# Kernel optimization log

Measured on AMD Instinct MI355X. Metric: run time of the kernel, lower is better.

Reference implementation:

```python
import jax, jax.numpy as jnp
import numpy as np

SCORE_THRESH = 0.05
NMS_THRESH = 0.5
DETS_PER_IMG = 100
IMG_W, IMG_H = 1333.0, 800.0
BBOX_XFORM_CLIP = float(np.log(1000.0 / 16.0))
WX, WY, WW, WH = 10.0, 10.0, 5.0, 5.0


def decode_boxes(rel, ref):
    widths = ref[:, 2] - ref[:, 0] + 1.0
    heights = ref[:, 3] - ref[:, 1] + 1.0
    ctr_x = ref[:, 0] + 0.5 * widths
    ctr_y = ref[:, 1] + 0.5 * heights
    dx = rel[:, 0] / WX
    dy = rel[:, 1] / WY
    dw = jnp.minimum(rel[:, 2] / WW, BBOX_XFORM_CLIP)
    dh = jnp.minimum(rel[:, 3] / WH, BBOX_XFORM_CLIP)
    pcx = dx * widths + ctr_x
    pcy = dy * heights + ctr_y
    pw = jnp.exp(dw) * widths
    ph = jnp.exp(dh) * heights
    return jnp.stack([pcx - 0.5 * pw, pcy - 0.5 * ph,
                      pcx + 0.5 * pw - 1.0, pcy + 0.5 * ph - 1.0], axis=1)


def pairwise_iou(b):
    # torchvision-style IoU (no +1), b: [n,4] xyxy
    area = (b[:, 2] - b[:, 0]) * (b[:, 3] - b[:, 1])
    lt = jnp.maximum(b[:, None, :2], b[None, :, :2])
    rb = jnp.minimum(b[:, None, 2:], b[None, :, 2:])
    wh = jnp.clip(rb - lt, 0.0)
    inter = wh[..., 0] * wh[..., 1]
    return inter / (area[:, None] + area[None, :] - inter + 1e-12)


def nms_keep(boxes, scores, valid):
    # masked greedy NMS; returns boolean keep mask in original order
    n = boxes.shape[0]
    order = jnp.argsort(-jnp.where(valid, scores, -jnp.inf))
    b = boxes[order]
    v = valid[order]
    iou = pairwise_iou(b)  # [n,n]
    idx = jnp.arange(n)

    def body(i, keep):
        suppressed = jnp.any(keep & (iou[i] > NMS_THRESH) & (idx < i))
        return keep.at[i].set(v[i] & ~suppressed)

    keep_sorted = jax.lax.fori_loop(0, n, body, jnp.zeros(n, dtype=bool))
    return jnp.zeros(n, dtype=bool).at[order].set(keep_sorted)


def setup_inputs() -> dict:
    key = jax.random.key(0)
    k1, k2, k3, k4, k5 = jax.random.split(key, 5)
    C, K = 16, 2048
    class_logit = jax.random.normal(k1, (C * K, 2), jnp.float32)
    box_regression = jax.random.normal(k2, (C * K, 8), jnp.float32) * 0.5
    x1 = jax.random.uniform(k3, (K,)) * (IMG_W - 220.0)
    y1 = jax.random.uniform(k4, (K,)) * (IMG_H - 220.0)
    wh = 20.0 + jax.random.uniform(k5, (K, 2)) * 180.0
    proposal_boxes = jnp.stack([x1, y1, x1 + wh[:, 0], y1 + wh[:, 1]], axis=1).astype(jnp.float32)
    unique_labels = jnp.arange(1, C + 1, dtype=jnp.int32)
    return {"class_logit": class_logit, "box_regression": box_regression,
            "proposal_boxes": proposal_boxes, "unique_labels": unique_labels}


def reference(class_logit, box_regression, proposal_boxes, unique_labels):
    C = unique_labels.shape[0]
    K = proposal_boxes.shape[0]
    # softmax over binary logits, take foreground prob
    prob = jax.nn.softmax(class_logit, axis=1)[:, 1]  # [C*K]
    rel = box_regression[:, 4:8]
    ref_boxes = jnp.tile(proposal_boxes, (C, 1))  # class-major [C*K,4]
    dec = decode_boxes(rel, ref_boxes)
    # clip_to_image (remove_empty=False), TO_REMOVE = 1
    dec = jnp.stack([jnp.clip(dec[:, 0], 0.0, IMG_W - 1.0),
                     jnp.clip(dec[:, 1], 0.0, IMG_H - 1.0),
                     jnp.clip(dec[:, 2], 0.0, IMG_W - 1.0),
                     jnp.clip(dec[:, 3], 0.0, IMG_H - 1.0)], axis=1)
    boxes_c = dec.reshape(C, K, 4)
    scores_c = prob.reshape(C, K)
    valid = scores_c > SCORE_THRESH
    keep = jax.vmap(nms_keep)(boxes_c, scores_c, valid).reshape(-1)  # [C*K]
    flat_scores = scores_c.reshape(-1)
    n_det = jnp.sum(keep)
    masked = jnp.where(keep, flat_scores, -jnp.inf)
    kth = jax.lax.top_k(masked, DETS_PER_IMG)[0][-1]  # 100th largest kept score
    keep_final = jnp.where(n_det > DETS_PER_IMG, keep & (flat_scores >= kth), keep)
    labels = jnp.broadcast_to(unique_labels[:, None], (C, K)).reshape(-1)
    out_boxes = jnp.where(keep_final[:, None], dec, 0.0)
    out_scores = jnp.where(keep_final, flat_scores, 0.0)
    out5 = jnp.concatenate([out_boxes, out_scores[:, None]], axis=1)  # [C*K,5]
    return out5, labels, keep_final
```

## Files before the change

### kernel.cpp

```cpp
#include <hip/hip_runtime.h>
#include <hip/hip_bf16.h>

#define NCLS 16
#define NBOX 2048
#define NTOT (NCLS * NBOX)
#define NCHUNK 32
#define SCORE_THRESH 0.05f
#define NMS_THRESH 0.5f
#define DETS_PER_IMG 100
#define TOPC 128
#define BBOX_CLIP 4.135166556742356f

typedef unsigned long long u64;

__device__ __forceinline__ u64 sel_mx(u64 a, u64 b, bool keepmax) {
    u64 mx = (a > b) ? a : b;
    u64 mn = (a > b) ? b : a;
    return keepmax ? mx : mn;
}

__global__ __launch_bounds__(1024) void sortmask_kernel(
    const float* __restrict__ logits,
    const float* __restrict__ regr,
    const float* __restrict__ props,
    float4* __restrict__ dec,
    u64* __restrict__ keys_out,
    u64* __restrict__ maskT)
{
    int blk = blockIdx.x;
    int c = blk >> 4;
    int p = blk & 15;
    int tid = threadIdx.x;

    int w = tid >> 6, l = tid & 63;
    int p0 = w * 128 + l;
    int p1 = p0 + 64;
    __shared__ float4 decv[NBOX];
    __shared__ float4 boxu[NBOX];
    u64* sk = (u64*)boxu;
    float4* box = boxu;

    u64 e01[2];
#pragma unroll
    for (int s = 0; s < 2; s++) {
#pragma clang fp contract(off)
        int t = s ? p1 : p0;
        int i = c * NBOX + t;
        float x0 = logits[2 * i + 0];
        float x1 = logits[2 * i + 1];
        float m = fmaxf(x0, x1);
        float e0f = expf(x0 - m);
        float e1f = expf(x1 - m);
        float score = e1f / (e0f + e1f);

        float px1 = props[4 * t + 0];
        float py1 = props[4 * t + 1];
        float px2 = props[4 * t + 2];
        float py2 = props[4 * t + 3];

        float bw = px2 - px1 + 1.0f;
        float bh = py2 - py1 + 1.0f;
        float cx = px1 + 0.5f * bw;
        float cy = py1 + 0.5f * bh;

        float dx = regr[8 * i + 4] / 10.0f;
        float dy = regr[8 * i + 5] / 10.0f;
        float dw = fminf(regr[8 * i + 6] / 5.0f, BBOX_CLIP);
        float dh = fminf(regr[8 * i + 7] / 5.0f, BBOX_CLIP);

        float pcx = dx * bw + cx;
        float pcy = dy * bh + cy;
        float pw  = expf(dw) * bw;
        float ph  = expf(dh) * bh;

        float b0 = pcx - 0.5f * pw;
        float b1 = pcy - 0.5f * ph;
        float b2 = pcx + 0.5f * pw - 1.0f;
        float b3 = pcy + 0.5f * ph - 1.0f;

        b0 = fminf(fmaxf(b0, 0.0f), 1332.0f);
        b1 = fminf(fmaxf(b1, 0.0f), 799.0f);
        b2 = fminf(fmaxf(b2, 0.0f), 1332.0f);
        b3 = fminf(fmaxf(b3, 0.0f), 799.0f);

        float4 bb = make_float4(b0, b1, b2, b3);
        decv[t] = bb;
        if (p == 0) dec[i] = bb;

        unsigned mono = 0u;
        if (score > SCORE_THRESH) mono = __float_as_uint(score) | 0x80000000u;
        e01[s] = ((u64)mono << 32) | (u64)(unsigned)(NBOX - 1 - t);
    }
    u64 e0 = e01[0], e1 = e01[1];

    for (int k = 2; k <= NBOX; k <<= 1) {
        bool desc0 = (p0 & k) == 0;
        bool desc1 = (p1 & k) == 0;
        for (int j = k >> 1; j > 0; j >>= 1) {
            if (j >= 128) {
                sk[p0] = e0; sk[p1] = e1;
                __syncthreads();
                u64 q0 = sk[p0 ^ j];
                u64 q1 = sk[p1 ^ j];
                e0 = sel_mx(e0, q0, desc0 ^ ((p0 & j) != 0));
                e1 = sel_mx(e1, q1, desc1 ^ ((p1 & j) != 0));
                __syncthreads();
            } else if (j == 64) {
                u64 mx = (e0 > e1) ? e0 : e1;
                u64 mn = (e0 > e1) ? e1 : e0;
                e0 = desc0 ? mx : mn;
                e1 = desc0 ? mn : mx;
            } else {
                u64 q0 = __shfl_xor(e0, j);
                u64 q1 = __shfl_xor(e1, j);
                bool hi = (l & j) != 0;
                e0 = sel_mx(e0, q0, desc0 ^ hi);
                e1 = sel_mx(e1, q1, desc1 ^ hi);
            }
        }
    }

    sk[p0] = e0; sk[p1] = e1;
    __syncthreads();

    u64 k0 = sk[tid];
    u64 k1 = sk[tid + 1024];
    if (p == 0) {
        keys_out[c * NBOX + tid] = k0;
        keys_out[c * NBOX + tid + 1024] = k1;
    }
    int i0 = (NBOX - 1) - (int)(k0 & 0xFFFFFFFFull);
    int i1 = (NBOX - 1) - (int)(k1 & 0xFFFFFFFFull);
    float4 g0 = decv[i0];
    float4 g1 = decv[i1];
    __syncthreads();
    box[tid] = g0;
    box[tid + 1024] = g1;
    __syncthreads();

    int r = tid & 63;
    int g = tid >> 6;

    for (int pass = 0; pass < 2; pass++) {
#pragma clang fp contract(off)
        int Jc = pass ? (31 - p) : p;
        int j = Jc * 64 + r;
        float4 jb = box[j];
        float jar = (jb.z - jb.x) * (jb.w - jb.y);
        float hj = 0.5f * jar;
        float colC = hj + 5e-13f;

        for (int I = g; I <= Jc; I += 16) {
            u64 wm = 0;
            int rbase = I * 64;
#pragma unroll
            for (int i2 = 0; i2 < 64; i2++) {
#pragma clang fp contract(off)
                int gi = rbase + i2;
                float4 rb = box[gi];
                float ar = (rb.z - rb.x) * (rb.w - rb.y);
                float rha = 0.5f * ar;
                float lx = fmaxf(rb.x, jb.x);
                float ly = fmaxf(rb.y, jb.y);
                float rx = fminf(rb.z, jb.z);
                float ry = fminf(rb.w, jb.w);
                float ww = fmaxf(rx - lx, 0.0f);
                float hh = fmaxf(ry - ly, 0.0f);
                float inter = ww * hh;
                float s  = rha + colC;
                float band = 2e-6f * s;
                float delta = fmaf(1.5f, inter, -s);
                bool over = delta > band;
                bool amb = fabsf(delta) <= band;
                if (__any(amb)) {
                    float un = ar + jar - inter + 1e-12f;
                    float iou = inter / un;
                    bool ovx = iou > NMS_THRESH;
                    over = amb ? ovx : over;
                }
                if (over) wm |= 1ull << i2;
            }
            if (I == Jc) wm &= (1ull << r) - 1ull;
            maskT[((size_t)c * NCHUNK + I) * NBOX + j] = wm;
        }
    }
}

__global__ __launch_bounds__(64) void resolve_kernel(
    const u64* __restrict__ keys,
    const u64* __restrict__ maskT,
    unsigned* __restrict__ keepbits,
    unsigned* __restrict__ compact,
    int* __restrict__ nkept)
{
    int c = blockIdx.x;
    int l = threadIdx.x;
    const u64* MT = maskT + (size_t)c * NCHUNK * NBOX;
    const u64* K  = keys + (size_t)c * NBOX;

    unsigned sup = 0;
    int offset = 0;
    u64 tm[2][NCHUNK - 1];

#pragma unroll
    for (int t = 0; t < NCHUNK - 1; t++)
        tm[0][t] = MT[(size_t)(1 + t) * 64 + l];
    u64 diag = MT[l];
    u64 key  = K[l];

#pragma unroll
    for (int I = 0; I < NCHUNK; I++) {
        u64 diagN = diag, keyN = key;
        if (I + 1 < NCHUNK) {
            const u64* rowpN = MT + (size_t)(I + 1) * NBOX + l;
#pragma unroll
            for (int t = 0; t < NCHUNK - 2 - I; t++)
                tm[(I + 1) & 1][t] = rowpN[(size_t)(I + 2 + t) * 64];
            diagN = MT[(size_t)(I + 1) * NBOX + (size_t)(I + 1) * 64 + l];
            keyN  = K[(I + 1) * 64 + l];
        }
        __builtin_amdgcn_sched_barrier(0);

        unsigned mono = (unsigned)(key >> 32);
        bool av = (mono != 0u) && (((sup >> I) & 1u) == 0u);
        u64 kept = 0;
        u64 availB = __ballot(av);
        while (availB) {
            u64 front = __ballot(av && ((diag & availB) == 0ull));
            kept |= front;
            bool fr = ((front >> l) & 1ull) != 0ull;
            bool sp = ((diag & front) != 0ull);
            av = av && !fr && !sp;
            availB = __ballot(av);
        }

        int idx = (NBOX - 1) - (int)(key & 0xFFFFFFFFull);
        bool isk = ((kept >> l) & 1ull) != 0ull;
        keepbits[c * NBOX + idx] = isk ? (mono & 0x7FFFFFFFu) : 0u;

        int pos = offset + __popcll(kept & ((1ull << l) - 1ull));
        if (isk && pos < TOPC) compact[c * TOPC + pos] = mono;
        offset += __popcll(kept);

#pragma unroll
        for (int t = 0; t < NCHUNK - 1 - I; t++)
            sup |= (tm[I & 1][t] & kept) ? (1u << (I + 1 + t)) : 0u;

        diag = diagN;
        key  = keyN;
    }

    for (int t = offset + l; t < TOPC; t += 64) compact[c * TOPC + t] = 0u;
    if (l == 0) nkept[c] = offset;
}

__global__ __launch_bounds__(256) void selectwrite_kernel(
    const unsigned* __restrict__ compact,
    const int* __restrict__ nkept,
    const unsigned* __restrict__ keepbits,
    const float4* __restrict__ dec,
    const int* __restrict__ ulabels,
    float* __restrict__ out)
{
    __shared__ unsigned ls[NCLS * TOPC];
    __shared__ int s_stats[2];
    int tid = threadIdx.x;

    for (int t = tid; t < NCLS * TOPC; t += 256) ls[t] = compact[t];
    __syncthreads();

    if (tid < 64) {
        int l = tid;
        int n_c = (l < NCLS) ? nkept[l] : 0;
        int nd = n_c;
#pragma unroll
        for (int off = 32; off > 0; off >>= 1) nd += __shfl_down(nd, off);
        nd = __shfl(nd, 0);

        unsigned kth = 0u;
        if (nd > DETS_PER_IMG) {
            const unsigned* my = &ls[(l & 15) * TOPC];
            bool active = (l < NCLS);
            unsigned prefix = 0u;
            for (int bit = 31; bit >= 0; bit--) {
                unsigned cand = prefix | (1u << bit);
                int cnt = 0;
                if (active) {
                    if (my[TOPC - 1] >= cand) cnt = TOPC;
                    else {
                        int pos = 0;
#pragma unroll
                        for (int step = 64; step >= 1; step >>= 1)
                            if (my[pos + step - 1] >= cand) pos += step;
                        cnt = pos;
                    }
                }
#pragma unroll
                for (int off = 32; off > 0; off >>= 1) cnt += __shfl_down(cnt, off);
                cnt = __shfl(cnt, 0);
                if (cnt >= DETS_PER_IMG) prefix = cand;
            }
            kth = prefix & 0x7FFFFFFFu;
        }
        if (l == 0) { s_stats[0] = nd; s_stats[1] = (int)kth; }
    }
    __syncthreads();

    int n_det = s_stats[0];
    unsigned kth = (unsigned)s_stats[1];

    int i = blockIdx.x * 256 + tid;
    unsigned kb = keepbits[i];
    bool kf = kb && (n_det <= DETS_PER_IMG || kb >= kth);

    float4 b = dec[i];
    float* o5 = out + (size_t)i * 5;
    if (kf) {
        o5[0] = b.x; o5[1] = b.y; o5[2] = b.z; o5[3] = b.w;
        o5[4] = __uint_as_float(kb);
    } else {
        o5[0] = 0.0f; o5[1] = 0.0f; o5[2] = 0.0f; o5[3] = 0.0f; o5[4] = 0.0f;
    }

    int c = i >> 11;
    out[NTOT * 5 + i] = (float)ulabels[c];
    out[NTOT * 5 + NTOT + i] = kf ? 1.0f : 0.0f;
}

extern "C" void kernel_launch(void* const* d_in, const int* in_sizes, int n_in,
                              void* d_out, int out_size, void* d_ws, size_t ws_size,
                              hipStream_t stream) {
    (void)in_sizes; (void)n_in; (void)out_size; (void)ws_size;

    const float* class_logit    = (const float*)d_in[0];
    const float* box_regression = (const float*)d_in[1];
    const float* proposal_boxes = (const float*)d_in[2];
    const int*   unique_labels  = (const int*)d_in[3];

    char* ws = (char*)d_ws;
    float4* dec        = (float4*)(ws + 0);
    u64* keys          = (u64*)(ws + 524288);
    u64* maskT         = (u64*)(ws + 786432);
    unsigned* keepbits = (unsigned*)(ws + 9175040);
    unsigned* compact  = (unsigned*)(ws + 9306112);
    int* nkept         = (int*)(ws + 9314304);

    float* out = (float*)d_out;

    sortmask_kernel<<<NCLS * 16, 1024, 0, stream>>>(class_logit, box_regression,
                                                    proposal_boxes, dec, keys,
                                                    maskT);
    resolve_kernel<<<NCLS, 64, 0, stream>>>(keys, maskT, keepbits,
                                            compact, nkept);
    selectwrite_kernel<<<NTOT / 256, 256, 0, stream>>>(compact, nkept, keepbits,
                                                       dec, unique_labels, out);
}
```

Before: 138.3 us.

## Replace cross-wave bitonic stages with per-wave sort plus merge-rank scatter

The full 2048-element bitonic sort now stops after the wave-local stages (each wave sorts 128 keys in registers and shuffles). The cross-wave stages, which needed many shared-memory round trips and barriers, are replaced by a rank computation: each element binary-searches all 16 sorted runs and counts the larger keys to find its final position, then scatters itself there. This removes most __syncthreads calls from the sort. In exchange each thread does 16 binary searches of 8 steps over shared memory, and the scheme depends on keys being unique, which the embedded index provides.

```diff
diff --git a/kernel.cpp b/kernel.cpp
--- a/kernel.cpp
+++ b/kernel.cpp
@@ -37,7 +37,7 @@
     int p1 = p0 + 64;
     __shared__ float4 decv[NBOX];
     __shared__ float4 boxu[NBOX];
-    u64* sk = (u64*)boxu;
+    u64* runs = (u64*)boxu;
     float4* box = boxu;
 
     u64 e01[2];
@@ -93,49 +93,60 @@
     }
     u64 e0 = e01[0], e1 = e01[1];
 
-    for (int k = 2; k <= NBOX; k <<= 1) {
-        bool desc0 = (p0 & k) == 0;
-        bool desc1 = (p1 & k) == 0;
+#pragma unroll
+    for (int k = 2; k <= 128; k <<= 1) {
+        bool d0 = ((l & k) == 0);
+        bool d1 = (((l + 64) & k) == 0);
+#pragma unroll
         for (int j = k >> 1; j > 0; j >>= 1) {
-            if (j >= 128) {
-                sk[p0] = e0; sk[p1] = e1;
-                __syncthreads();
-                u64 q0 = sk[p0 ^ j];
-                u64 q1 = sk[p1 ^ j];
-                e0 = sel_mx(e0, q0, desc0 ^ ((p0 & j) != 0));
-                e1 = sel_mx(e1, q1, desc1 ^ ((p1 & j) != 0));
-                __syncthreads();
-            } else if (j == 64) {
+            if (j == 64) {
                 u64 mx = (e0 > e1) ? e0 : e1;
                 u64 mn = (e0 > e1) ? e1 : e0;
-                e0 = desc0 ? mx : mn;
-                e1 = desc0 ? mn : mx;
+                e0 = d0 ? mx : mn;
+                e1 = d0 ? mn : mx;
             } else {
                 u64 q0 = __shfl_xor(e0, j);
                 u64 q1 = __shfl_xor(e1, j);
                 bool hi = (l & j) != 0;
-                e0 = sel_mx(e0, q0, desc0 ^ hi);
-                e1 = sel_mx(e1, q1, desc1 ^ hi);
+                e0 = sel_mx(e0, q0, d0 ^ hi);
+                e1 = sel_mx(e1, q1, d1 ^ hi);
             }
         }
     }
 
-    sk[p0] = e0; sk[p1] = e1;
-    __syncthreads();
-
-    u64 k0 = sk[tid];
-    u64 k1 = sk[tid + 1024];
-    if (p == 0) {
-        keys_out[c * NBOX + tid] = k0;
-        keys_out[c * NBOX + tid + 1024] = k1;
-    }
-    int i0 = (NBOX - 1) - (int)(k0 & 0xFFFFFFFFull);
-    int i1 = (NBOX - 1) - (int)(k1 & 0xFFFFFFFFull);
+    runs[w * 128 + l] = e0;
+    runs[w * 128 + 64 + l] = e1;
+    __syncthreads();
+
+    int rank0 = 0, rank1 = 0;
+#pragma unroll
+    for (int R = 0; R < 16; R++) {
+        const u64* run = runs + R * 128;
+        int pa = 0, pb = 0;
+#pragma unroll
+        for (int step = 128; step >= 1; step >>= 1) {
+            int qa = pa + step - 1;
+            int qb = pb + step - 1;
+            u64 va = run[qa & 127];
+            u64 vb = run[qb & 127];
+            if (qa < 128 && va > e0) pa += step;
+            if (qb < 128 && vb > e1) pb += step;
+        }
+        rank0 += pa;
+        rank1 += pb;
+    }
+
+    int i0 = (NBOX - 1) - (int)(e0 & 0xFFFFFFFFull);
+    int i1 = (NBOX - 1) - (int)(e1 & 0xFFFFFFFFull);
     float4 g0 = decv[i0];
     float4 g1 = decv[i1];
-    __syncthreads();
-    box[tid] = g0;
-    box[tid + 1024] = g1;
+    if (p == 0) {
+        keys_out[c * NBOX + rank0] = e0;
+        keys_out[c * NBOX + rank1] = e1;
+    }
+    __syncthreads();
+    box[rank0] = g0;
+    box[rank1] = g1;
     __syncthreads();
 
     int r = tid & 63;
```

Result: no change. 136.4 us (-1.4%).
